# Performance work log

Measured on AMD Instinct MI355X. Metric: run time of the kernel, lower is better.

## Reference

```python
import math
import jax, jax.numpy as jnp
import numpy as np

N = 100000
E = 800000
IN_DIM = 128
HID = 128
HEADS = 4
C = HID // HEADS  # 32 per-head channels
TD = 16           # time encoding dim
NL = 2            # layers - 1 conv blocks
OUT = 2
BN_EPS = 1e-5


def setup_inputs() -> dict:
    key = jax.random.key(0)
    ks = jax.random.split(key, 24)
    s = 0.05
    inp = {
        "x": jax.random.normal(ks[0], (N, IN_DIM), dtype=jnp.float32),
        "edge_index": jax.random.randint(ks[1], (2, E), 0, N, dtype=jnp.int32),
        "timesteps": jax.random.randint(ks[2], (N,), 0, 100000, dtype=jnp.int32),
        # input projection Linear(in_dim + td, hid)
        "proj_w": jax.random.normal(ks[3], (IN_DIM + TD, HID), dtype=jnp.float32) * s,
        "proj_b": jnp.zeros((HID,), dtype=jnp.float32),
        # GATConv params per layer (stacked over NL layers)
        "conv_w": jax.random.normal(ks[4], (NL, HID, HID), dtype=jnp.float32) * s,
        "conv_b": jnp.zeros((NL, HID), dtype=jnp.float32),
        "att_src": jax.random.normal(ks[5], (NL, HEADS, C), dtype=jnp.float32) * s,
        "att_dst": jax.random.normal(ks[6], (NL, HEADS, C), dtype=jnp.float32) * s,
        # BatchNorm (eval mode: running stats)
        "bn_gamma": jax.random.uniform(ks[7], (NL, HID), dtype=jnp.float32) + 0.5,
        "bn_beta": jax.random.normal(ks[8], (NL, HID), dtype=jnp.float32) * s,
        "bn_mean": jax.random.normal(ks[9], (NL, HID), dtype=jnp.float32) * s,
        "bn_var": jax.random.uniform(ks[10], (NL, HID), dtype=jnp.float32) + 0.5,
        # age gate MLP: Linear(1,16) -> ReLU -> Linear(16,1) -> Sigmoid
        "gate_w1": jax.random.normal(ks[11], (1, 16), dtype=jnp.float32) * 0.5,
        "gate_b1": jnp.zeros((16,), dtype=jnp.float32),
        "gate_w2": jax.random.normal(ks[12], (16, 1), dtype=jnp.float32) * 0.5,
        "gate_b2": jnp.zeros((1,), dtype=jnp.float32),
        # head: Linear(hid, hid//2) -> ReLU -> Linear(hid//2, out)
        "head_w1": jax.random.normal(ks[13], (HID, HID // 2), dtype=jnp.float32) * s,
        "head_b1": jnp.zeros((HID // 2,), dtype=jnp.float32),
        "head_w2": jax.random.normal(ks[14], (HID // 2, OUT), dtype=jnp.float32) * s,
        "head_b2": jnp.zeros((OUT,), dtype=jnp.float32),
    }
    return inp


def _time_enc(t):
    # t: [N] float -> [N, TD] sinusoidal encoding
    t = t[:, None]
    freqs = jnp.exp(jnp.arange(0, TD, 2, dtype=jnp.float32) * (-(math.log(10000.0) / TD)))
    return jnp.concatenate([jnp.sin(t * freqs), jnp.cos(t * freqs)], axis=-1)


def _gat_conv(h_in, src, dst, W, b, a_src, a_dst):
    # h_in: [N, HID]; src/dst: [Etot] with self-loops included
    h = (h_in @ W).reshape(N, HEADS, C)                 # [N, H, C]
    al_s = jnp.sum(h * a_src[None], axis=-1)            # [N, H]
    al_d = jnp.sum(h * a_dst[None], axis=-1)            # [N, H]
    alpha = jax.nn.leaky_relu(al_s[src] + al_d[dst], 0.2)  # [Etot, H]
    # segment softmax over destination nodes
    m = jax.ops.segment_max(alpha, dst, num_segments=N)    # [N, H]
    ex = jnp.exp(alpha - m[dst])
    den = jax.ops.segment_sum(ex, dst, num_segments=N)     # [N, H]
    att = ex / (den[dst] + 1e-16)                          # [Etot, H]
    msg = h[src] * att[:, :, None]                         # [Etot, H, C]
    out = jax.ops.segment_sum(msg, dst, num_segments=N)    # [N, H, C]
    return out.reshape(N, HID) + b


def reference(x, edge_index, timesteps, proj_w, proj_b, conv_w, conv_b,
              att_src, att_dst, bn_gamma, bn_beta, bn_mean, bn_var,
              gate_w1, gate_b1, gate_w2, gate_b2,
              head_w1, head_b1, head_w2, head_b2):
    t = timesteps.astype(jnp.float32)
    te = _time_enc(t)                                      # [N, TD]
    h = jax.nn.relu(jnp.concatenate([x, te], axis=-1) @ proj_w + proj_b)
    # ages in [0, 1]
    mn, mx = jnp.min(t), jnp.max(t)
    ages = ((t - mn) / jnp.maximum(mx - mn, 1.0))[:, None]  # [N, 1]
    gate = jax.nn.sigmoid(jax.nn.relu(ages @ gate_w1 + gate_b1) @ gate_w2 + gate_b2)  # [N, 1]
    # add self-loops (PyG GATConv default)
    loop = jnp.arange(N, dtype=edge_index.dtype)
    src = jnp.concatenate([edge_index[0], loop])
    dst = jnp.concatenate([edge_index[1], loop])
    for i in range(NL):
        h = _gat_conv(h, src, dst, conv_w[i], conv_b[i], att_src[i], att_dst[i])
        h = (h - bn_mean[i]) * (bn_gamma[i] / jnp.sqrt(bn_var[i] + BN_EPS)) + bn_beta[i]
        h = jax.nn.elu(h)
        h = h * gate  # dropout is identity in eval mode
    h = jax.nn.relu(h @ head_w1 + head_b1)
    return h @ head_w2 + head_b2  # [N, OUT]
```

## Files before the change

kernel.cpp:

```cpp
#include <hip/hip_runtime.h>
#include <cfloat>
#include <climits>
#include <cmath>

constexpr int N_ = 100000;
constexpr int E_ = 800000;
constexpr int NBLK_ = (N_ + 255) / 256;

__global__ __launch_bounds__(256) void k_prep(const int* __restrict__ ts, float* __restrict__ te,
                                              int* __restrict__ count, int* __restrict__ bmin,
                                              int* __restrict__ bmax) {
    const float FRQ[8] = {1.0f, 0.31622776601683794f, 0.1f, 0.031622776601683794f,
                          0.01f, 0.0031622776601683794f, 0.001f, 0.00031622776601683794f};
    int n = blockIdx.x * 256 + threadIdx.x;
    int tv_min = INT_MAX, tv_max = INT_MIN;
    if (n < N_) {
        int tv = ts[n];
        tv_min = tv; tv_max = tv;
        count[n] = 1;
        float tf = (float)tv;
#pragma unroll
        for (int j = 0; j < 8; ++j) {
            float sv, cv;
            sincosf(tf * FRQ[j], &sv, &cv);
            te[n * 16 + j] = sv;
            te[n * 16 + 8 + j] = cv;
        }
    }
#pragma unroll
    for (int o = 32; o >= 1; o >>= 1) {
        tv_min = min(tv_min, __shfl_xor(tv_min, o));
        tv_max = max(tv_max, __shfl_xor(tv_max, o));
    }
    __shared__ int smn[4], smx[4];
    if ((threadIdx.x & 63) == 0) {
        smn[threadIdx.x >> 6] = tv_min;
        smx[threadIdx.x >> 6] = tv_max;
    }
    __syncthreads();
    if (threadIdx.x == 0) {
        bmin[blockIdx.x] = min(min(smn[0], smn[1]), min(smn[2], smn[3]));
        bmax[blockIdx.x] = max(max(smx[0], smx[1]), max(smx[2], smx[3]));
    }
}

__global__ __launch_bounds__(256) void k_count(const int* __restrict__ ei, int* __restrict__ count) {
    int e = blockIdx.x * 256 + threadIdx.x;
    if (e < E_) atomicAdd(&count[ei[E_ + e]], 1);
}

__global__ __launch_bounds__(256) void k_bsum(const int* __restrict__ count, int* __restrict__ bsum) {
    int i = blockIdx.x * 256 + threadIdx.x;
    int v = (i < N_) ? count[i] : 0;
#pragma unroll
    for (int o = 32; o >= 1; o >>= 1) v += __shfl_xor(v, o);
    __shared__ int wsum[4];
    if ((threadIdx.x & 63) == 0) wsum[threadIdx.x >> 6] = v;
    __syncthreads();
    if (threadIdx.x == 0) bsum[blockIdx.x] = wsum[0] + wsum[1] + wsum[2] + wsum[3];
}

__global__ __launch_bounds__(512) void k_bscan(int* __restrict__ bsum, int* __restrict__ indptr,
                                               const int* __restrict__ bmin, const int* __restrict__ bmax,
                                               int* __restrict__ minmax) {
    int t = threadIdx.x;
    int v = (t < NBLK_) ? bsum[t] : 0;
    __shared__ int sc[512];
    sc[t] = v;
    __syncthreads();
    for (int o = 1; o < 512; o <<= 1) {
        int u = (t >= o) ? sc[t - o] : 0;
        __syncthreads();
        sc[t] += u;
        __syncthreads();
    }
    if (t < NBLK_) bsum[t] = sc[t] - v;
    if (t == NBLK_ - 1) indptr[N_] = sc[t];
    int mn = (t < NBLK_) ? bmin[t] : INT_MAX;
    int mx = (t < NBLK_) ? bmax[t] : INT_MIN;
#pragma unroll
    for (int o = 32; o >= 1; o >>= 1) {
        mn = min(mn, __shfl_xor(mn, o));
        mx = max(mx, __shfl_xor(mx, o));
    }
    __shared__ int rmn[8], rmx[8];
    if ((t & 63) == 0) { rmn[t >> 6] = mn; rmx[t >> 6] = mx; }
    __syncthreads();
    if (t == 0) {
        int a = INT_MAX, b = INT_MIN;
#pragma unroll
        for (int q = 0; q < 8; ++q) { a = min(a, rmn[q]); b = max(b, rmx[q]); }
        minmax[0] = a;
        minmax[1] = b;
    }
}

__global__ __launch_bounds__(256) void k_scan_c(const int* __restrict__ count, const int* __restrict__ bsum,
                                                int* __restrict__ indptr, int* __restrict__ srcs,
                                                int* __restrict__ cursor, const int* __restrict__ ts,
                                                const int* __restrict__ minmax, const float* __restrict__ gw1,
                                                const float* __restrict__ gb1, const float* __restrict__ gw2,
                                                const float* __restrict__ gb2, float* __restrict__ gate) {
    int t = threadIdx.x;
    int i = blockIdx.x * 256 + t;
    int v = (i < N_) ? count[i] : 0;
    __shared__ int sc[256];
    sc[t] = v;
    __syncthreads();
    for (int o = 1; o < 256; o <<= 1) {
        int u = (t >= o) ? sc[t - o] : 0;
        __syncthreads();
        sc[t] += u;
        __syncthreads();
    }
    if (i < N_) {
        int off = bsum[blockIdx.x] + sc[t] - v;
        indptr[i] = off;
        srcs[off] = i;
        cursor[i] = off + 1;
        float mn = (float)minmax[0], mx = (float)minmax[1];
        float age = ((float)ts[i] - mn) / fmaxf(mx - mn, 1.0f);
        float o2 = gb2[0];
#pragma unroll
        for (int j = 0; j < 16; ++j) {
            float hj = fmaxf(age * gw1[j] + gb1[j], 0.f);
            o2 += hj * gw2[j];
        }
        gate[i] = 1.f / (1.f + __expf(-o2));
    }
}

__global__ __launch_bounds__(256) void k_scatter(const int* __restrict__ ei, int* __restrict__ cursor,
                                                 int* __restrict__ srcs) {
    int e = blockIdx.x * 256 + threadIdx.x;
    if (e < E_) {
        int s = ei[e];
        int d = ei[E_ + e];
        int p = atomicAdd(&cursor[d], 1);
        srcs[p] = s;
    }
}

template <int K, int M, int MODE>
__global__ __launch_bounds__((M / 4) * 16) void k_gemm(const float* __restrict__ A, const float* __restrict__ te,
                                                       const float* __restrict__ W, const float* __restrict__ bias,
                                                       const float* __restrict__ asrc, const float* __restrict__ adst,
                                                       const float* __restrict__ w2, const float* __restrict__ b2,
                                                       float* __restrict__ Cout, float* __restrict__ al_s,
                                                       float* __restrict__ al_d) {
    constexpr int GR = 128, KC = 16;
    constexpr int CTH = M / 4;
    constexpr int TB = CTH * 16;
    constexpr int NA = (GR * KC / 4) / TB;
    constexpr int NW = (KC * M / 4) / TB;
    __shared__ float As[KC][GR + 4];
    __shared__ float Ws[KC][M];
    __shared__ float asl[128], adl[128];
    __shared__ float w2l[128];
    const int r0 = blockIdx.x * GR;
    const int tid = threadIdx.x;
    const int tx = tid % CTH, ty = tid / CTH;
    if (MODE == 1 && tid < 128) { asl[tid] = asrc[tid]; adl[tid] = adst[tid]; }
    if (MODE == 2 && tid < 128) { w2l[tid] = w2[tid]; }
    float acc[8][4];
#pragma unroll
    for (int i = 0; i < 8; ++i)
#pragma unroll
        for (int j = 0; j < 4; ++j) acc[i][j] = 0.f;

    for (int k0 = 0; k0 < K; k0 += KC) {
        __syncthreads();
#pragma unroll
        for (int i = 0; i < NA; ++i) {
            int f = tid + i * TB;
            int row = f >> 2, fq = f & 3;
            int gr = r0 + row;
            float4 v = make_float4(0.f, 0.f, 0.f, 0.f);
            if (gr < N_) {
                if (MODE == 0) {
                    if (k0 < 128) v = *(const float4*)&A[gr * 128 + k0 + fq * 4];
                    else          v = *(const float4*)&te[gr * 16 + fq * 4];
                } else {
                    v = *(const float4*)&A[gr * K + k0 + fq * 4];
                }
            }
            As[fq * 4 + 0][row] = v.x;
            As[fq * 4 + 1][row] = v.y;
            As[fq * 4 + 2][row] = v.z;
            As[fq * 4 + 3][row] = v.w;
        }
#pragma unroll
        for (int i = 0; i < NW; ++i) {
            int f = tid + i * TB;
            int kk = f / (M / 4), c4 = f % (M / 4);
            *(float4*)&Ws[kk][c4 * 4] = *(const float4*)&W[(k0 + kk) * M + c4 * 4];
        }
        __syncthreads();
#pragma unroll
        for (int kk = 0; kk < KC; ++kk) {
            float4 a0 = *(const float4*)&As[kk][ty * 8];
            float4 a1 = *(const float4*)&As[kk][ty * 8 + 4];
            float av[8] = {a0.x, a0.y, a0.z, a0.w, a1.x, a1.y, a1.z, a1.w};
            float4 w = *(const float4*)&Ws[kk][tx * 4];
            float wv[4] = {w.x, w.y, w.z, w.w};
#pragma unroll
            for (int i = 0; i < 8; ++i)
#pragma unroll
                for (int j = 0; j < 4; ++j) acc[i][j] = fmaf(av[i], wv[j], acc[i][j]);
        }
    }

#pragma unroll
    for (int i = 0; i < 8; ++i) {
        int gr = r0 + ty * 8 + i;
        bool valid = gr < N_;
        if (MODE == 0) {
            if (valid) {
                float4 v;
                v.x = fmaxf(acc[i][0] + bias[tx * 4 + 0], 0.f);
                v.y = fmaxf(acc[i][1] + bias[tx * 4 + 1], 0.f);
                v.z = fmaxf(acc[i][2] + bias[tx * 4 + 2], 0.f);
                v.w = fmaxf(acc[i][3] + bias[tx * 4 + 3], 0.f);
                *(float4*)&Cout[gr * M + tx * 4] = v;
            }
        } else if (MODE == 1) {
            if (valid) {
                float4 v = make_float4(acc[i][0], acc[i][1], acc[i][2], acc[i][3]);
                *(float4*)&Cout[gr * M + tx * 4] = v;
            }
            float ps = 0.f, pd = 0.f;
#pragma unroll
            for (int q = 0; q < 4; ++q) {
                int c = tx * 4 + q;
                ps = fmaf(acc[i][q], asl[c], ps);
                pd = fmaf(acc[i][q], adl[c], pd);
            }
#pragma unroll
            for (int o = 1; o <= 4; o <<= 1) {
                ps += __shfl_xor(ps, o);
                pd += __shfl_xor(pd, o);
            }
            if (valid && (tx & 7) == 0) {
                int head = tx >> 3;
                al_s[gr * 4 + head] = ps;
                al_d[gr * 4 + head] = pd;
            }
        } else {
            float ps0 = 0.f, ps1 = 0.f;
#pragma unroll
            for (int q = 0; q < 4; ++q) {
                float hv = fmaxf(acc[i][q] + bias[tx * 4 + q], 0.f);
                int c = tx * 4 + q;
                ps0 = fmaf(hv, w2l[c * 2 + 0], ps0);
                ps1 = fmaf(hv, w2l[c * 2 + 1], ps1);
            }
#pragma unroll
            for (int o = 1; o <= 8; o <<= 1) {
                ps0 += __shfl_xor(ps0, o);
                ps1 += __shfl_xor(ps1, o);
            }
            if (valid && tx == 0) {
                *(float2*)&Cout[gr * 2] = make_float2(ps0 + b2[0], ps1 + b2[1]);
            }
        }
    }
}

__global__ __launch_bounds__(256) void k_gat(const int* __restrict__ indptr, const int* __restrict__ srcs,
                                             const float* __restrict__ al_s, const float* __restrict__ al_d,
                                             const float* __restrict__ h2, const float* __restrict__ convb,
                                             const float* __restrict__ gamma, const float* __restrict__ beta,
                                             const float* __restrict__ mean, const float* __restrict__ var,
                                             const float* __restrict__ gate, float* __restrict__ hout) {
    int g = threadIdx.x >> 4, lg = threadIdx.x & 15;
    int n = blockIdx.x * 16 + g;
    if (n >= N_) return;
    int start = indptr[n], end = indptr[n + 1];
    int hl = lg >> 2;
    int c0 = lg * 8;
    float gn = gate[n];
    float4 ad4 = *(const float4*)&al_d[n * 4];
    float adv[4] = {ad4.x, ad4.y, ad4.z, ad4.w};
    float M[4] = {-FLT_MAX, -FLT_MAX, -FLT_MAX, -FLT_MAX};
    float D[4] = {0.f, 0.f, 0.f, 0.f};
    float ac[8] = {0.f, 0.f, 0.f, 0.f, 0.f, 0.f, 0.f, 0.f};

    for (int p0 = start; p0 < end; p0 += 16) {
        int cs = end - p0;
        if (cs > 16) cs = 16;
        float a[4];
        int s = 0;
        if (lg < cs) {
            s = srcs[p0 + lg];
            float4 as4 = *(const float4*)&al_s[s * 4];
            float asv[4] = {as4.x, as4.y, as4.z, as4.w};
#pragma unroll
            for (int h = 0; h < 4; ++h) {
                float x = asv[h] + adv[h];
                a[h] = x > 0.f ? x : 0.2f * x;
            }
        } else {
#pragma unroll
            for (int h = 0; h < 4; ++h) a[h] = -FLT_MAX;
        }
        float f[4], w[4];
#pragma unroll
        for (int h = 0; h < 4; ++h) {
            float m = a[h];
#pragma unroll
            for (int o = 8; o >= 1; o >>= 1) m = fmaxf(m, __shfl_xor(m, o));
            float Mn = fmaxf(M[h], m);
            f[h] = __expf(M[h] - Mn);
            M[h] = Mn;
            w[h] = __expf(a[h] - Mn);
            float sv = w[h];
#pragma unroll
            for (int o = 8; o >= 1; o >>= 1) sv += __shfl_xor(sv, o);
            D[h] = D[h] * f[h] + sv;
        }
        float fh = hl < 2 ? (hl == 0 ? f[0] : f[1]) : (hl == 2 ? f[2] : f[3]);
        float whl = hl < 2 ? (hl == 0 ? w[0] : w[1]) : (hl == 2 ? w[2] : w[3]);
#pragma unroll
        for (int q = 0; q < 8; ++q) ac[q] *= fh;
        int i = 0;
        for (; i + 1 < cs; i += 2) {
            float w0 = __shfl(whl, i, 16);
            float w1 = __shfl(whl, i + 1, 16);
            int s0 = __shfl(s, i, 16);
            int s1 = __shfl(s, i + 1, 16);
            float4 h0a = *(const float4*)&h2[s0 * 128 + c0];
            float4 h0b = *(const float4*)&h2[s0 * 128 + c0 + 4];
            float4 h1a = *(const float4*)&h2[s1 * 128 + c0];
            float4 h1b = *(const float4*)&h2[s1 * 128 + c0 + 4];
            ac[0] = fmaf(w0, h0a.x, ac[0]); ac[1] = fmaf(w0, h0a.y, ac[1]);
            ac[2] = fmaf(w0, h0a.z, ac[2]); ac[3] = fmaf(w0, h0a.w, ac[3]);
            ac[4] = fmaf(w0, h0b.x, ac[4]); ac[5] = fmaf(w0, h0b.y, ac[5]);
            ac[6] = fmaf(w0, h0b.z, ac[6]); ac[7] = fmaf(w0, h0b.w, ac[7]);
            ac[0] = fmaf(w1, h1a.x, ac[0]); ac[1] = fmaf(w1, h1a.y, ac[1]);
            ac[2] = fmaf(w1, h1a.z, ac[2]); ac[3] = fmaf(w1, h1a.w, ac[3]);
            ac[4] = fmaf(w1, h1b.x, ac[4]); ac[5] = fmaf(w1, h1b.y, ac[5]);
            ac[6] = fmaf(w1, h1b.z, ac[6]); ac[7] = fmaf(w1, h1b.w, ac[7]);
        }
        if (i < cs) {
            float w0 = __shfl(whl, i, 16);
            int s0 = __shfl(s, i, 16);
            float4 h0a = *(const float4*)&h2[s0 * 128 + c0];
            float4 h0b = *(const float4*)&h2[s0 * 128 + c0 + 4];
            ac[0] = fmaf(w0, h0a.x, ac[0]); ac[1] = fmaf(w0, h0a.y, ac[1]);
            ac[2] = fmaf(w0, h0a.z, ac[2]); ac[3] = fmaf(w0, h0a.w, ac[3]);
            ac[4] = fmaf(w0, h0b.x, ac[4]); ac[5] = fmaf(w0, h0b.y, ac[5]);
            ac[6] = fmaf(w0, h0b.z, ac[6]); ac[7] = fmaf(w0, h0b.w, ac[7]);
        }
    }

    float Dh = hl < 2 ? (hl == 0 ? D[0] : D[1]) : (hl == 2 ? D[2] : D[3]);
    float rd = 1.0f / (Dh + 1e-16f);
    float out8[8];
#pragma unroll
    for (int half = 0; half < 2; ++half) {
        int cb0 = c0 + half * 4;
        float4 cb = *(const float4*)&convb[cb0];
        float4 gm = *(const float4*)&gamma[cb0];
        float4 bt = *(const float4*)&beta[cb0];
        float4 mu = *(const float4*)&mean[cb0];
        float4 vr = *(const float4*)&var[cb0];
        float cbv[4] = {cb.x, cb.y, cb.z, cb.w};
        float gmv[4] = {gm.x, gm.y, gm.z, gm.w};
        float btv[4] = {bt.x, bt.y, bt.z, bt.w};
        float muv[4] = {mu.x, mu.y, mu.z, mu.w};
        float vrv[4] = {vr.x, vr.y, vr.z, vr.w};
#pragma unroll
        for (int q = 0; q < 4; ++q) {
            float val = ac[half * 4 + q] * rd + cbv[q];
            float sc = gmv[q] * rsqrtf(vrv[q] + 1e-5f);
            val = (val - muv[q]) * sc + btv[q];
            val = val > 0.f ? val : expm1f(val);
            out8[half * 4 + q] = val * gn;
        }
    }
    *(float4*)&hout[n * 128 + c0] = make_float4(out8[0], out8[1], out8[2], out8[3]);
    *(float4*)&hout[n * 128 + c0 + 4] = make_float4(out8[4], out8[5], out8[6], out8[7]);
}

extern "C" void kernel_launch(void* const* d_in, const int* in_sizes, int n_in,
                              void* d_out, int out_size, void* d_ws, size_t ws_size,
                              hipStream_t stream) {
    const float* x       = (const float*)d_in[0];
    const int*   ei      = (const int*)d_in[1];
    const int*   ts      = (const int*)d_in[2];
    const float* proj_w  = (const float*)d_in[3];
    const float* proj_b  = (const float*)d_in[4];
    const float* conv_w  = (const float*)d_in[5];
    const float* conv_b  = (const float*)d_in[6];
    const float* att_src = (const float*)d_in[7];
    const float* att_dst = (const float*)d_in[8];
    const float* bn_g    = (const float*)d_in[9];
    const float* bn_b    = (const float*)d_in[10];
    const float* bn_m    = (const float*)d_in[11];
    const float* bn_v    = (const float*)d_in[12];
    const float* gw1     = (const float*)d_in[13];
    const float* gb1     = (const float*)d_in[14];
    const float* gw2     = (const float*)d_in[15];
    const float* gb2     = (const float*)d_in[16];
    const float* hw1     = (const float*)d_in[17];
    const float* hb1     = (const float*)d_in[18];
    const float* hw2     = (const float*)d_in[19];
    const float* hb2     = (const float*)d_in[20];
    float* out = (float*)d_out;

    float* ws   = (float*)d_ws;
    float* h    = ws;
    float* h2   = h + (size_t)N_ * 128;
    float* te   = h2 + (size_t)N_ * 128;
    float* al_s = te + (size_t)N_ * 16;
    float* al_d = al_s + (size_t)N_ * 4;
    float* gate = al_d + (size_t)N_ * 4;
    int* indptr = (int*)(gate + N_);
    int* srcs   = indptr + (N_ + 1);
    int* count  = srcs + (N_ + E_);
    int* cursor = count + N_;
    int* bsum   = cursor + N_;
    int* bmin   = bsum + NBLK_;
    int* bmax   = bmin + NBLK_;
    int* minmax = bmax + NBLK_;

    k_prep<<<NBLK_, 256, 0, stream>>>(ts, te, count, bmin, bmax);
    k_count<<<(E_ + 255) / 256, 256, 0, stream>>>(ei, count);
    k_bsum<<<NBLK_, 256, 0, stream>>>(count, bsum);
    k_bscan<<<1, 512, 0, stream>>>(bsum, indptr, bmin, bmax, minmax);
    k_scan_c<<<NBLK_, 256, 0, stream>>>(count, bsum, indptr, srcs, cursor, ts, minmax,
                                        gw1, gb1, gw2, gb2, gate);
    k_scatter<<<(E_ + 255) / 256, 256, 0, stream>>>(ei, cursor, srcs);

    k_gemm<144, 128, 0><<<782, 512, 0, stream>>>(x, te, proj_w, proj_b, nullptr, nullptr,
                                                 nullptr, nullptr, h, nullptr, nullptr);
    for (int l = 0; l < 2; ++l) {
        k_gemm<128, 128, 1><<<782, 512, 0, stream>>>(h, nullptr, conv_w + l * 128 * 128, nullptr,
                                                     att_src + l * 128, att_dst + l * 128,
                                                     nullptr, nullptr, h2, al_s, al_d);
        k_gat<<<(N_ + 15) / 16, 256, 0, stream>>>(indptr, srcs, al_s, al_d, h2, conv_b + l * 128,
                                                  bn_g + l * 128, bn_b + l * 128, bn_m + l * 128,
                                                  bn_v + l * 128, gate, h);
    }
    k_gemm<128, 64, 2><<<782, 256, 0, stream>>>(h, nullptr, hw1, hb1, nullptr, nullptr,
                                                hw2, hb2, out, nullptr, nullptr);
}
```

Baseline: 463.2 us.

## Register-prefetch next K-chunk in GEMM, widen KC, unroll GAT gather by four

The tiled GEMM now loads the next K chunk from global memory into registers while computing on the current shared-memory tile, then stores it to shared memory after a barrier. This hides global-load latency behind the FMA work. KC becomes a template parameter, raised to 32 for the conv and head GEMMs to halve the number of barrier rounds, at the cost of more shared memory and registers. The GAT aggregation loop gains a 4-way unrolled gather so more neighbour-row loads are in flight at once.

```diff
diff --git a/kernel.cpp b/kernel.cpp
--- a/kernel.cpp
+++ b/kernel.cpp
@@ -141,18 +141,21 @@
     }
 }
 
-template <int K, int M, int MODE>
+template <int K, int M, int KC, int MODE>
 __global__ __launch_bounds__((M / 4) * 16) void k_gemm(const float* __restrict__ A, const float* __restrict__ te,
                                                        const float* __restrict__ W, const float* __restrict__ bias,
                                                        const float* __restrict__ asrc, const float* __restrict__ adst,
                                                        const float* __restrict__ w2, const float* __restrict__ b2,
                                                        float* __restrict__ Cout, float* __restrict__ al_s,
                                                        float* __restrict__ al_d) {
-    constexpr int GR = 128, KC = 16;
+    constexpr int GR = 128;
     constexpr int CTH = M / 4;
     constexpr int TB = CTH * 16;
     constexpr int NA = (GR * KC / 4) / TB;
     constexpr int NW = (KC * M / 4) / TB;
+    constexpr int F4R = KC / 4;
+    constexpr int NCH = K / KC;
+    static_assert(K % KC == 0, "K%KC");
     __shared__ float As[KC][GR + 4];
     __shared__ float Ws[KC][M];
     __shared__ float asl[128], adl[128];
@@ -168,34 +171,57 @@
 #pragma unroll
         for (int j = 0; j < 4; ++j) acc[i][j] = 0.f;
 
-    for (int k0 = 0; k0 < K; k0 += KC) {
-        __syncthreads();
+    float4 pa[NA], pw[NW];
+
+    auto LDG = [&](int c) {
+        const int k0 = c * KC;
 #pragma unroll
         for (int i = 0; i < NA; ++i) {
             int f = tid + i * TB;
-            int row = f >> 2, fq = f & 3;
+            int row = f / F4R, fq = f % F4R;
             int gr = r0 + row;
             float4 v = make_float4(0.f, 0.f, 0.f, 0.f);
             if (gr < N_) {
                 if (MODE == 0) {
-                    if (k0 < 128) v = *(const float4*)&A[gr * 128 + k0 + fq * 4];
-                    else          v = *(const float4*)&te[gr * 16 + fq * 4];
+                    int kg = k0 + fq * 4;
+                    if (kg < 128) v = *(const float4*)&A[gr * 128 + kg];
+                    else          v = *(const float4*)&te[gr * 16 + (kg - 128)];
                 } else {
                     v = *(const float4*)&A[gr * K + k0 + fq * 4];
                 }
             }
-            As[fq * 4 + 0][row] = v.x;
-            As[fq * 4 + 1][row] = v.y;
-            As[fq * 4 + 2][row] = v.z;
-            As[fq * 4 + 3][row] = v.w;
+            pa[i] = v;
         }
 #pragma unroll
         for (int i = 0; i < NW; ++i) {
             int f = tid + i * TB;
             int kk = f / (M / 4), c4 = f % (M / 4);
-            *(float4*)&Ws[kk][c4 * 4] = *(const float4*)&W[(k0 + kk) * M + c4 * 4];
-        }
-        __syncthreads();
+            pw[i] = *(const float4*)&W[(k0 + kk) * M + c4 * 4];
+        }
+    };
+    auto STS = [&]() {
+#pragma unroll
+        for (int i = 0; i < NA; ++i) {
+            int f = tid + i * TB;
+            int row = f / F4R, fq = f % F4R;
+            As[fq * 4 + 0][row] = pa[i].x;
+            As[fq * 4 + 1][row] = pa[i].y;
+            As[fq * 4 + 2][row] = pa[i].z;
+            As[fq * 4 + 3][row] = pa[i].w;
+        }
+#pragma unroll
+        for (int i = 0; i < NW; ++i) {
+            int f = tid + i * TB;
+            int kk = f / (M / 4), c4 = f % (M / 4);
+            *(float4*)&Ws[kk][c4 * 4] = pw[i];
+        }
+    };
+
+    LDG(0);
+    STS();
+    __syncthreads();
+    for (int c = 0; c < NCH; ++c) {
+        if (c + 1 < NCH) LDG(c + 1);
 #pragma unroll
         for (int kk = 0; kk < KC; ++kk) {
             float4 a0 = *(const float4*)&As[kk][ty * 8];
@@ -207,6 +233,11 @@
             for (int i = 0; i < 8; ++i)
 #pragma unroll
                 for (int j = 0; j < 4; ++j) acc[i][j] = fmaf(av[i], wv[j], acc[i][j]);
+        }
+        if (c + 1 < NCH) {
+            __syncthreads();
+            STS();
+            __syncthreads();
         }
     }
 
@@ -323,6 +354,40 @@
 #pragma unroll
         for (int q = 0; q < 8; ++q) ac[q] *= fh;
         int i = 0;
+        for (; i + 3 < cs; i += 4) {
+            float w0 = __shfl(whl, i, 16);
+            float w1 = __shfl(whl, i + 1, 16);
+            float w2 = __shfl(whl, i + 2, 16);
+            float w3 = __shfl(whl, i + 3, 16);
+            int s0 = __shfl(s, i, 16);
+            int s1 = __shfl(s, i + 1, 16);
+            int s2 = __shfl(s, i + 2, 16);
+            int s3 = __shfl(s, i + 3, 16);
+            float4 h0a = *(const float4*)&h2[s0 * 128 + c0];
+            float4 h0b = *(const float4*)&h2[s0 * 128 + c0 + 4];
+            float4 h1a = *(const float4*)&h2[s1 * 128 + c0];
+            float4 h1b = *(const float4*)&h2[s1 * 128 + c0 + 4];
+            float4 h2a = *(const float4*)&h2[s2 * 128 + c0];
+            float4 h2b = *(const float4*)&h2[s2 * 128 + c0 + 4];
+            float4 h3a = *(const float4*)&h2[s3 * 128 + c0];
+            float4 h3b = *(const float4*)&h2[s3 * 128 + c0 + 4];
+            ac[0] = fmaf(w0, h0a.x, ac[0]); ac[1] = fmaf(w0, h0a.y, ac[1]);
+            ac[2] = fmaf(w0, h0a.z, ac[2]); ac[3] = fmaf(w0, h0a.w, ac[3]);
+            ac[4] = fmaf(w0, h0b.x, ac[4]); ac[5] = fmaf(w0, h0b.y, ac[5]);
+            ac[6] = fmaf(w0, h0b.z, ac[6]); ac[7] = fmaf(w0, h0b.w, ac[7]);
+            ac[0] = fmaf(w1, h1a.x, ac[0]); ac[1] = fmaf(w1, h1a.y, ac[1]);
+            ac[2] = fmaf(w1, h1a.z, ac[2]); ac[3] = fmaf(w1, h1a.w, ac[3]);
+            ac[4] = fmaf(w1, h1b.x, ac[4]); ac[5] = fmaf(w1, h1b.y, ac[5]);
+            ac[6] = fmaf(w1, h1b.z, ac[6]); ac[7] = fmaf(w1, h1b.w, ac[7]);
+            ac[0] = fmaf(w2, h2a.x, ac[0]); ac[1] = fmaf(w2, h2a.y, ac[1]);
+            ac[2] = fmaf(w2, h2a.z, ac[2]); ac[3] = fmaf(w2, h2a.w, ac[3]);
+            ac[4] = fmaf(w2, h2b.x, ac[4]); ac[5] = fmaf(w2, h2b.y, ac[5]);
+            ac[6] = fmaf(w2, h2b.z, ac[6]); ac[7] = fmaf(w2, h2b.w, ac[7]);
+            ac[0] = fmaf(w3, h3a.x, ac[0]); ac[1] = fmaf(w3, h3a.y, ac[1]);
+            ac[2] = fmaf(w3, h3a.z, ac[2]); ac[3] = fmaf(w3, h3a.w, ac[3]);
+            ac[4] = fmaf(w3, h3b.x, ac[4]); ac[5] = fmaf(w3, h3b.y, ac[5]);
+            ac[6] = fmaf(w3, h3b.z, ac[6]); ac[7] = fmaf(w3, h3b.w, ac[7]);
+        }
         for (; i + 1 < cs; i += 2) {
             float w0 = __shfl(whl, i, 16);
             float w1 = __shfl(whl, i + 1, 16);
@@ -432,16 +497,16 @@
                                         gw1, gb1, gw2, gb2, gate);
     k_scatter<<<(E_ + 255) / 256, 256, 0, stream>>>(ei, cursor, srcs);
 
-    k_gemm<144, 128, 0><<<782, 512, 0, stream>>>(x, te, proj_w, proj_b, nullptr, nullptr,
-                                                 nullptr, nullptr, h, nullptr, nullptr);
+    k_gemm<144, 128, 16, 0><<<782, 512, 0, stream>>>(x, te, proj_w, proj_b, nullptr, nullptr,
+                                                     nullptr, nullptr, h, nullptr, nullptr);
     for (int l = 0; l < 2; ++l) {
-        k_gemm<128, 128, 1><<<782, 512, 0, stream>>>(h, nullptr, conv_w + l * 128 * 128, nullptr,
-                                                     att_src + l * 128, att_dst + l * 128,
-                                                     nullptr, nullptr, h2, al_s, al_d);
+        k_gemm<128, 128, 32, 1><<<782, 512, 0, stream>>>(h, nullptr, conv_w + l * 128 * 128, nullptr,
+                                                         att_src + l * 128, att_dst + l * 128,
+                                                         nullptr, nullptr, h2, al_s, al_d);
         k_gat<<<(N_ + 15) / 16, 256, 0, stream>>>(indptr, srcs, al_s, al_d, h2, conv_b + l * 128,
                                                   bn_g + l * 128, bn_b + l * 128, bn_m + l * 128,
                                                   bn_v + l * 128, gate, h);
     }
-    k_gemm<128, 64, 2><<<782, 256, 0, stream>>>(h, nullptr, hw1, hb1, nullptr, nullptr,
-                                                hw2, hb2, out, nullptr, nullptr);
-}
+    k_gemm<128, 64, 32, 2><<<782, 256, 0, stream>>>(h, nullptr, hw1, hb1, nullptr, nullptr,
+                                                    hw2, hb2, out, nullptr, nullptr);
+}
```

Result: slower. 1.326 ms (+186.3%).
